# Performance work log

Measured on AMD Instinct MI355X. Metric: run time of the kernel, lower is better.

Reference implementation:

```python
import jax, jax.numpy as jnp
import numpy as np
from jax.scipy.special import digamma

# Dims (see init_kwargs): pose P=4 -> D=16, stem A=128, primary caps B=32,
# classes C=10, class-caps kernel K=6 (== primary feature map size), 3 routing iters.
P, D, A, B, C, K, ITER = 4, 16, 128, 32, 10, 6, 3
N = B * K * K                                    # input capsules routed to each class capsule
ALPHA0, KAPPA0, NU0 = 1.0, 1.0, float(D + 1)     # Dirichlet/Normal-Wishart priors (m0=0, Psi0=I, cov='diag')
BN_EPS, EPS = 1e-5, 1e-8


def conv2d(x, w, s):
    return jax.lax.conv_general_dilated(x, w, (s, s), 'VALID',
                                        dimension_numbers=('NCHW', 'OIHW', 'NCHW'))


def bn(x, gamma, beta, axes):
    # batch-norm with batch statistics (training-mode math)
    mu = x.mean(axes, keepdims=True)
    var = x.var(axes, keepdims=True)
    return (x - mu) * jax.lax.rsqrt(var + BN_EPS) * gamma + beta


def setup_inputs():
    key = jax.random.key(0)
    ks = jax.random.split(key, 4)
    f32 = jnp.float32
    x = jax.random.normal(ks[0], (128, 3, 32, 32), dtype=f32)
    conv1_w = jax.random.normal(ks[1], (A, 3, 5, 5), dtype=f32) * 0.1
    bn1_g = jnp.ones((A,), f32); bn1_b = jnp.zeros((A,), f32)
    prim_w = jax.random.normal(ks[2], (B * D + B, A, 3, 3), dtype=f32) * 0.05
    bna_g = jnp.ones((B,), f32); bna_b = jnp.zeros((B,), f32)
    bnp_g = jnp.ones((B,), f32); bnp_b = jnp.zeros((B,), f32)
    W_ij = jax.random.normal(ks[3], (B, C, K, K, P, P), dtype=f32) * 0.3
    return dict(x=x, conv1_w=conv1_w, bn1_g=bn1_g, bn1_b=bn1_b, prim_w=prim_w,
                bna_g=bna_g, bna_b=bna_b, bnp_g=bnp_g, bnp_b=bnp_b, W_ij=W_ij)


def _vb_stats(Ra, V):
    # Ra: (b,N,C) responsibility * input activation; V: (b,N,C,D) votes
    Nj = Ra.sum(1) + EPS                                         # (b,C)
    xbar = jnp.einsum('bnc,bncd->bcd', Ra, V) / Nj[..., None]    # weighted vote mean
    diff = V - xbar[:, None]
    sigma = jnp.einsum('bnc,bncd->bcd', Ra, diff * diff) / Nj[..., None]  # diag cov
    kappa = KAPPA0 + Nj
    m = Nj[..., None] * xbar / kappa[..., None]                  # posterior mean (m0 = 0)
    nu = NU0 + Nj
    Psi = 1.0 + Nj[..., None] * sigma + (KAPPA0 * Nj / kappa)[..., None] * xbar * xbar  # Psi0 = I (diag)
    return Nj, kappa, m, nu, Psi


def _expectations(Nj, nu, Psi, d_idx):
    alpha = ALPHA0 + Nj
    E_lnpi = digamma(alpha) - digamma(alpha.sum(-1, keepdims=True))
    E_lnLam = (digamma(0.5 * (nu[..., None] + 1.0 - d_idx)).sum(-1)
               + D * jnp.log(2.0) - jnp.log(Psi).sum(-1))
    return E_lnpi, E_lnLam


def reference(x, conv1_w, bn1_g, bn1_b, prim_w, bna_g, bna_b, bnp_g, bnp_b, W_ij):
    b = x.shape[0]
    # --- stem: Conv5x5/s2 + BN + ReLU ---
    h = conv2d(x, conv1_w, 2)                                    # (b,A,14,14)
    h = jax.nn.relu(bn(h, bn1_g[None, :, None, None], bn1_b[None, :, None, None], (0, 2, 3)))
    # --- primary capsules: Conv3x3/s2 -> poses + activations ---
    pc = conv2d(h, prim_w, 2)                                    # (b,B*D+B,6,6)
    poses, a = pc[:, :B * D], pc[:, B * D:]
    a = jax.nn.sigmoid(bn(a, bna_g[None, :, None, None], bna_b[None, :, None, None], (0, 2, 3)))
    poses = bn(poses.reshape(b, B, D, K, K),
               bnp_g[None, :, None, None, None], bnp_b[None, :, None, None, None], (0, 2, 3, 4))
    poses = poses.reshape(b, B, P, P, K, K)
    # --- class capsules: votes V = W_ij @ pose, kernel covers whole 6x6 map ---
    V = jnp.einsum('icxypq,biqrxy->bicxypr', W_ij, poses)        # (b,B,C,K,K,P,P)
    V = V.transpose(0, 1, 3, 4, 2, 5, 6).reshape(b, N, C, D)
    a_i = a.reshape(b, N)
    # --- variational Bayes routing (diag Normal-Wishart, ITER iterations) ---
    d_idx = jnp.arange(1, D + 1, dtype=x.dtype)
    R = jnp.full((b, N, C), 1.0 / C, dtype=x.dtype)
    for t in range(ITER):
        Nj, kappa, m, nu, Psi = _vb_stats(R * a_i[:, :, None], V)
        if t < ITER - 1:
            E_lnpi, E_lnLam = _expectations(Nj, nu, Psi, d_idx)
            dm = V - m[:, None]
            quad = D / kappa[:, None, :] + nu[:, None, :] * jnp.einsum('bncd,bcd->bnc', dm * dm, 1.0 / Psi)
            lnp = (E_lnpi[:, None] + 0.5 * E_lnLam[:, None]
                   - 0.5 * D * jnp.log(2.0 * jnp.pi) - 0.5 * quad)
            R = jax.nn.softmax(lnp, axis=-1)
    E_lnpi, E_lnLam = _expectations(Nj, nu, Psi, d_idx)
    logits = E_lnpi + 0.5 * E_lnLam                              # (b,C)
    yhat = jax.nn.sigmoid(bn(logits, 1.0, 0.0, (0,)))            # BatchNorm1d(affine=False)
    return yhat
```

## Files before the change

### kernel.cpp

```cpp
#include <hip/hip_runtime.h>
#include <hip/hip_bf16.h>

#define NB 128
#define AA 128
#define BB 32
#define CC 10
#define KK 6
#define DD 16
#define NN 1152
#define H1 14
#define CH2 544
#define NG 4608
#define KG 1152
#define MG 576

typedef short bfrag8 __attribute__((ext_vector_type(8)));
typedef float facc4 __attribute__((ext_vector_type(4)));

__device__ __forceinline__ unsigned short f2bf(float f) {
    unsigned u = __float_as_uint(f);
    u += 0x7FFF + ((u >> 16) & 1);
    return (unsigned short)(u >> 16);
}
__device__ __forceinline__ float bf2f(unsigned short s) {
    return __uint_as_float(((unsigned)s) << 16);
}

__global__ __launch_bounds__(256, 3) void k_conv1(const float* __restrict__ x,
                                                  const float* __restrict__ w,
                                                  float* __restrict__ h) {
    __shared__ __align__(16) float sX[3][7][32];
    __shared__ float sWf[AA * 75];
    const int p = blockIdx.x;
    const int b = blockIdx.y;
    const int tid = threadIdx.x;
    for (int j = tid; j < AA * 75; j += 256) sWf[j] = w[j];
    for (int j = tid; j < 3 * 7 * 32; j += 256) {
        int col = j & 31; int t2 = j >> 5; int row = t2 % 7; int ic = t2 / 7;
        sX[ic][row][col] = x[b * 3072 + ic * 1024 + (4 * p + row) * 32 + col];
    }
    __syncthreads();
    const int oc = tid & 127, ry = tid >> 7;
    const int r = 2 * p + ry;
    float acc[14];
#pragma unroll
    for (int j = 0; j < 14; ++j) acc[j] = 0.f;
    const float* wr = sWf + oc * 75;
#pragma unroll
    for (int ic = 0; ic < 3; ++ic) {
#pragma unroll
        for (int ky = 0; ky < 5; ++ky) {
            const float* xr = &sX[ic][2 * ry + ky][0];
            float row[32];
#pragma unroll
            for (int q = 0; q < 8; ++q) {
                float4 v = *reinterpret_cast<const float4*>(xr + q * 4);
                row[q * 4 + 0] = v.x; row[q * 4 + 1] = v.y;
                row[q * 4 + 2] = v.z; row[q * 4 + 3] = v.w;
            }
            float w0 = wr[ic * 25 + ky * 5 + 0];
            float w1 = wr[ic * 25 + ky * 5 + 1];
            float w2 = wr[ic * 25 + ky * 5 + 2];
            float w3 = wr[ic * 25 + ky * 5 + 3];
            float w4 = wr[ic * 25 + ky * 5 + 4];
#pragma unroll
            for (int ox = 0; ox < 14; ++ox) {
                float s = acc[ox];
                s = fmaf(row[2 * ox + 0], w0, s);
                s = fmaf(row[2 * ox + 1], w1, s);
                s = fmaf(row[2 * ox + 2], w2, s);
                s = fmaf(row[2 * ox + 3], w3, s);
                s = fmaf(row[2 * ox + 4], w4, s);
                acc[ox] = s;
            }
        }
    }
    float* out = h + ((size_t)(b * AA + oc) * 14 + r) * 14;
#pragma unroll
    for (int q = 0; q < 7; ++q)
        *reinterpret_cast<float2*>(out + q * 2) = make_float2(acc[q * 2], acc[q * 2 + 1]);
}

__device__ __forceinline__ void blk_reduce2(float& s, float& s2, int tid) {
#pragma unroll
    for (int o = 32; o > 0; o >>= 1) { s += __shfl_down(s, o); s2 += __shfl_down(s2, o); }
    __shared__ float ls[4], lq[4];
    int lane = tid & 63, wid = tid >> 6;
    if (lane == 0) { ls[wid] = s; lq[wid] = s2; }
    __syncthreads();
    if (tid == 0) {
        s = ls[0] + ls[1] + ls[2] + ls[3];
        s2 = lq[0] + lq[1] + lq[2] + lq[3];
    }
}

__global__ void k_bnstats1a(const float* __restrict__ h, float* __restrict__ part) {
    int c = blockIdx.x & 127, sl = blockIdx.x >> 7;
    int tid = threadIdx.x;
    float s = 0.f, s2 = 0.f;
    for (int j = tid; j < 16 * 196; j += 256) {
        int b = sl * 16 + j / 196, hw = j % 196;
        float v = h[((size_t)b * AA + c) * 196 + hw];
        s += v; s2 += v * v;
    }
    blk_reduce2(s, s2, tid);
    if (tid == 0) { part[c * 8 + sl] = s; part[1024 + c * 8 + sl] = s2; }
}

__global__ void k_bnfin1(const float* __restrict__ part, const float* __restrict__ g,
                         const float* __restrict__ be, float* __restrict__ bn1) {
    int c = threadIdx.x;
    float s = 0.f, s2 = 0.f;
#pragma unroll
    for (int sl = 0; sl < 8; ++sl) { s += part[c * 8 + sl]; s2 += part[1024 + c * 8 + sl]; }
    const float n = (float)(NB * 196);
    float mu = s / n;
    float var = s2 / n - mu * mu;
    float sc = g[c] * rsqrtf(var + 1e-5f);
    bn1[c] = sc;
    bn1[AA + c] = be[c] - mu * sc;
}

__global__ void k_prepw(const float* __restrict__ w, unsigned short* __restrict__ Ah,
                        unsigned short* __restrict__ Al) {
    int t = blockIdx.x * 256 + threadIdx.x;
    if (t >= MG * (KG / 8)) return;
    int row = t / (KG / 8), seg = t % (KG / 8);
    alignas(16) unsigned short hi[8], lo[8];
    if (row < CH2) {
        const float* src = w + (size_t)row * KG + seg * 8;
#pragma unroll
        for (int j = 0; j < 8; ++j) {
            float v = src[j];
            unsigned short hh = f2bf(v);
            hi[j] = hh;
            lo[j] = f2bf(v - bf2f(hh));
        }
    } else {
#pragma unroll
        for (int j = 0; j < 8; ++j) { hi[j] = 0; lo[j] = 0; }
    }
    *reinterpret_cast<uint4*>(Ah + (size_t)row * KG + seg * 8) = *reinterpret_cast<const uint4*>(hi);
    *reinterpret_cast<uint4*>(Al + (size_t)row * KG + seg * 8) = *reinterpret_cast<const uint4*>(lo);
}

__global__ void k_im2col(const float* __restrict__ h, const float* __restrict__ bn1,
                         unsigned short* __restrict__ Bh, unsigned short* __restrict__ Bl) {
    int t = blockIdx.x * 256 + threadIdx.x;
    if (t >= NG * (KG / 8)) return;
    int n = t / (KG / 8), seg = t % (KG / 8);
    int b = n / 36, xy = n % 36;
    int oy = xy / 6, ox = xy % 6;
    const float* hb = h + (size_t)b * (AA * 196) + (2 * oy) * 14 + 2 * ox;
    alignas(16) unsigned short hi[8], lo[8];
#pragma unroll
    for (int j = 0; j < 8; ++j) {
        int k = seg * 8 + j;
        int ic = k / 9, kk = k - ic * 9;
        int ky = kk / 3, kx = kk - ky * 3;
        float v = hb[ic * 196 + ky * 14 + kx];
        v = fmaxf(fmaf(v, bn1[ic], bn1[AA + ic]), 0.f);
        unsigned short hh = f2bf(v);
        hi[j] = hh;
        lo[j] = f2bf(v - bf2f(hh));
    }
    *reinterpret_cast<uint4*>(Bh + (size_t)n * KG + seg * 8) = *reinterpret_cast<const uint4*>(hi);
    *reinterpret_cast<uint4*>(Bl + (size_t)n * KG + seg * 8) = *reinterpret_cast<const uint4*>(lo);
}

__global__ __launch_bounds__(256, 4) void k_gemm(const unsigned short* __restrict__ Ah,
                                                 const unsigned short* __restrict__ Al,
                                                 const unsigned short* __restrict__ Bh,
                                                 const unsigned short* __restrict__ Bl,
                                                 float* __restrict__ pcT) {
    __shared__ alignas(16) unsigned short sAh[64][44], sAl[64][44];
    __shared__ alignas(16) unsigned short sBh[64][44], sBl[64][44];
    const int s = blockIdx.x;
    const int k8 = s & 7, j = s >> 3;
    const int jm = j / 9;
    const int y = k8 + 8 * jm;
    const int xg = j - 9 * jm;
    const int oc0 = xg * 64;
    const int n0 = y * 64;
    const int tid = threadIdx.x;
    const int lane = tid & 63, wv = tid >> 6;
    const int wm = wv >> 1, wn = wv & 1;
    const int quad = lane >> 4, r16 = lane & 15;
    const int srow = tid >> 2, sseg = tid & 3;

    facc4 acc[2][2] = {};
    const size_t gA = (size_t)(oc0 + srow) * KG + sseg * 8;
    const size_t gB = (size_t)(n0 + srow) * KG + sseg * 8;

    for (int ks = 0; ks < KG / 32; ++ks) {
        const int k0 = ks * 32;
        uint4 vAh = *reinterpret_cast<const uint4*>(Ah + gA + k0);
        uint4 vAl = *reinterpret_cast<const uint4*>(Al + gA + k0);
        uint4 vBh = *reinterpret_cast<const uint4*>(Bh + gB + k0);
        uint4 vBl = *reinterpret_cast<const uint4*>(Bl + gB + k0);
        __syncthreads();
        *reinterpret_cast<uint4*>(&sAh[srow][sseg * 8]) = vAh;
        *reinterpret_cast<uint4*>(&sAl[srow][sseg * 8]) = vAl;
        *reinterpret_cast<uint4*>(&sBh[srow][sseg * 8]) = vBh;
        *reinterpret_cast<uint4*>(&sBl[srow][sseg * 8]) = vBl;
        __syncthreads();
        bfrag8 ah[2], al[2], bh[2], bl[2];
#pragma unroll
        for (int i = 0; i < 2; ++i) {
            ah[i] = *reinterpret_cast<const bfrag8*>(&sAh[wm * 32 + i * 16 + r16][quad * 8]);
            al[i] = *reinterpret_cast<const bfrag8*>(&sAl[wm * 32 + i * 16 + r16][quad * 8]);
            bh[i] = *reinterpret_cast<const bfrag8*>(&sBh[wn * 32 + i * 16 + r16][quad * 8]);
            bl[i] = *reinterpret_cast<const bfrag8*>(&sBl[wn * 32 + i * 16 + r16][quad * 8]);
        }
#pragma unroll
        for (int i = 0; i < 2; ++i)
#pragma unroll
            for (int jj = 0; jj < 2; ++jj) {
                acc[i][jj] = __builtin_amdgcn_mfma_f32_16x16x32_bf16(ah[i], bh[jj], acc[i][jj], 0, 0, 0);
                acc[i][jj] = __builtin_amdgcn_mfma_f32_16x16x32_bf16(ah[i], bl[jj], acc[i][jj], 0, 0, 0);
                acc[i][jj] = __builtin_amdgcn_mfma_f32_16x16x32_bf16(al[i], bh[jj], acc[i][jj], 0, 0, 0);
            }
    }
#pragma unroll
    for (int i = 0; i < 2; ++i) {
        int oc_base = oc0 + wm * 32 + i * 16 + quad * 4;
        if (oc_base >= CH2) continue;
#pragma unroll
        for (int jj = 0; jj < 2; ++jj) {
            int n = n0 + wn * 32 + jj * 16 + r16;
            *reinterpret_cast<facc4*>(pcT + (size_t)n * CH2 + oc_base) = acc[i][jj];
        }
    }
}

__global__ void k_bnstats2a(const float* __restrict__ pcT, float* __restrict__ part) {
    int blk = blockIdx.x, tid = threadIdx.x;
    float s = 0.f, s2 = 0.f;
    if (blk < 256) {
        int i = blk >> 3, sl = blk & 7;
        for (int j = tid; j < 576 * 4; j += 256) {
            int row = sl * 576 + (j >> 2), q = j & 3;
            float4 v = *reinterpret_cast<const float4*>(pcT + (size_t)row * CH2 + i * 16 + q * 4);
            s += v.x + v.y + v.z + v.w;
            s2 += v.x * v.x + v.y * v.y + v.z * v.z + v.w * v.w;
        }
        blk_reduce2(s, s2, tid);
        if (tid == 0) { part[blk] = s; part[256 + blk] = s2; }
    } else {
        int t2 = blk - 256;
        int ch = t2 >> 1, sl = t2 & 1;
        for (int j = tid; j < 2304; j += 256) {
            int row = sl * 2304 + j;
            float v = pcT[(size_t)row * CH2 + BB * DD + ch];
            s += v; s2 += v * v;
        }
        blk_reduce2(s, s2, tid);
        if (tid == 0) { part[512 + t2] = s; part[576 + t2] = s2; }
    }
}

__global__ void k_bnfin2(const float* __restrict__ part,
                         const float* __restrict__ bna_g, const float* __restrict__ bna_b,
                         const float* __restrict__ bnp_g, const float* __restrict__ bnp_b,
                         float* __restrict__ bn2) {
    int t = threadIdx.x;
    if (t < 32) {
        float s = 0.f, s2 = 0.f;
#pragma unroll
        for (int sl = 0; sl < 8; ++sl) { s += part[t * 8 + sl]; s2 += part[256 + t * 8 + sl]; }
        const float n = (float)(NB * DD * 36);
        float mu = s / n, var = s2 / n - mu * mu;
        float sc = bnp_g[t] * rsqrtf(var + 1e-5f);
        bn2[t] = sc; bn2[32 + t] = bnp_b[t] - mu * sc;
    } else {
        int ch = t - 32;
        float s = part[512 + ch * 2] + part[512 + ch * 2 + 1];
        float s2 = part[576 + ch * 2] + part[576 + ch * 2 + 1];
        const float n = (float)(NB * 36);
        float mu = s / n, var = s2 / n - mu * mu;
        float sc = bna_g[ch] * rsqrtf(var + 1e-5f);
        bn2[64 + ch] = sc; bn2[96 + ch] = bna_b[ch] - mu * sc;
    }
}

template <int FIRST>
__global__ __launch_bounds__(640) void k_routed(
    const float* __restrict__ pcT, const float* __restrict__ bn2,
    const float* __restrict__ Wij, const float* __restrict__ m,
    const float* __restrict__ G, const float* __restrict__ base,
    float* __restrict__ S0p, float* __restrict__ S1p, float* __restrict__ S2p) {
    const int b = blockIdx.x >> 1, half = blockIdx.x & 1;
    const int tid = threadIdx.x;
    const int c = tid >> 6, lane = tid & 63;
    __shared__ float sLnp[2][CC][65];
    __shared__ float sBn2[128];
    if (tid < 128) sBn2[tid] = bn2[tid];
    float mc[16], Gc[16], basec = 0.f;
    if (!FIRST) {
        int bc16 = (b * CC + c) * 16;
#pragma unroll
        for (int d = 0; d < 16; ++d) { mc[d] = m[bc16 + d]; Gc[d] = G[bc16 + d]; }
        basec = base[b * CC + c];
    }
    float s0 = 0.f, s1[16], s2[16];
#pragma unroll
    for (int d = 0; d < 16; ++d) { s1[d] = 0.f; s2[d] = 0.f; }
    __syncthreads();

#pragma unroll 1
    for (int it = 0; it < 9; ++it) {
        const int n = half * 576 + it * 64 + lane;
        const int i = n / 36, xy = n - i * 36;
        const int row = b * 36 + xy;
        const float4* pp = reinterpret_cast<const float4*>(pcT + (size_t)row * CH2 + i * 16);
        const float4* wp = reinterpret_cast<const float4*>(Wij + (((size_t)i * CC + c) * 36 + xy) * 16);
        alignas(16) float P[16], W[16];
        *reinterpret_cast<float4*>(&P[0])  = pp[0];
        *reinterpret_cast<float4*>(&P[4])  = pp[1];
        *reinterpret_cast<float4*>(&P[8])  = pp[2];
        *reinterpret_cast<float4*>(&P[12]) = pp[3];
        *reinterpret_cast<float4*>(&W[0])  = wp[0];
        *reinterpret_cast<float4*>(&W[4])  = wp[1];
        *reinterpret_cast<float4*>(&W[8])  = wp[2];
        *reinterpret_cast<float4*>(&W[12]) = wp[3];
        const float psc = sBn2[i], psh = sBn2[32 + i];
#pragma unroll
        for (int d = 0; d < 16; ++d) P[d] = fmaf(P[d], psc, psh);
        float V[16];
#pragma unroll
        for (int p = 0; p < 4; ++p)
#pragma unroll
            for (int r = 0; r < 4; ++r)
                V[p * 4 + r] = W[p * 4 + 0] * P[0 + r] + W[p * 4 + 1] * P[4 + r] +
                               W[p * 4 + 2] * P[8 + r] + W[p * 4 + 3] * P[12 + r];
        float va = fmaf(pcT[(size_t)row * CH2 + BB * DD + i], sBn2[64 + i], sBn2[96 + i]);
        float av = 1.f / (1.f + expf(-va));
        float wgt;
        if (FIRST) {
            wgt = 0.1f * av;
        } else {
            float q = 0.f;
#pragma unroll
            for (int d = 0; d < 16; ++d) {
                float dm = V[d] - mc[d];
                q = fmaf(dm * dm, Gc[d], q);
            }
            float lnp = basec - q;
            sLnp[it & 1][c][lane] = lnp;
            __syncthreads();
            float mx = -1e30f;
#pragma unroll
            for (int cc = 0; cc < CC; ++cc) mx = fmaxf(mx, sLnp[it & 1][cc][lane]);
            float ssum = 0.f;
#pragma unroll
            for (int cc = 0; cc < CC; ++cc) ssum += expf(sLnp[it & 1][cc][lane] - mx);
            wgt = expf(lnp - mx) / ssum * av;
        }
        s0 += wgt;
#pragma unroll
        for (int d = 0; d < 16; ++d) {
            float wv = wgt * V[d];
            s1[d] += wv;
            s2[d] = fmaf(wv, V[d], s2[d]);
        }
    }
#pragma unroll
    for (int o = 32; o > 0; o >>= 1) {
        s0 += __shfl_down(s0, o);
#pragma unroll
        for (int k = 0; k < 16; ++k) {
            s1[k] += __shfl_down(s1[k], o);
            s2[k] += __shfl_down(s2[k], o);
        }
    }
    if (lane == 0) {
        int idx = half * (NB * CC) + b * CC + c;
        S0p[idx] = s0;
#pragma unroll
        for (int k = 0; k < 16; ++k) { S1p[idx * 16 + k] = s1[k]; S2p[idx * 16 + k] = s2[k]; }
    }
}

__device__ __forceinline__ float digammaf_(float x) {
    float r = 0.f;
    while (x < 6.f) { r -= 1.f / x; x += 1.f; }
    float xi = 1.f / x;
    float xi2 = xi * xi;
    return r + logf(x) - 0.5f * xi -
           xi2 * (0.0833333333f - xi2 * (0.0083333333f - xi2 * 0.0039682540f));
}

template <int LOGITS>
__global__ void k_expect(const float* __restrict__ S0p, const float* __restrict__ S1p,
                         const float* __restrict__ S2p, float* __restrict__ m,
                         float* __restrict__ G, float* __restrict__ base,
                         float* __restrict__ logits) {
    int b = blockIdx.x;
    int c = threadIdx.x;
    __shared__ float alph[CC];
    float njraw = 0.f;
    if (c < CC) {
        njraw = S0p[b * CC + c] + S0p[NB * CC + b * CC + c];
        alph[c] = 1.f + njraw + 1e-8f;
    }
    __syncthreads();
    if (c < CC) {
        int bc = b * CC + c;
        float nj = njraw + 1e-8f;
        float asum = 0.f;
#pragma unroll
        for (int k = 0; k < CC; ++k) asum += alph[k];
        float kappa = 1.f + nj;
        float nu = 17.f + nj;
        float S0 = njraw;
        float elnlam = 16.f * 0.69314718056f;
        for (int d = 0; d < 16; ++d) {
            float s1 = S1p[bc * 16 + d] + S1p[(NB * CC + bc) * 16 + d];
            float s2v = S2p[bc * 16 + d] + S2p[(NB * CC + bc) * 16 + d];
            float xbar = s1 / nj;
            float sig = (s2v - 2.f * xbar * s1 + xbar * xbar * S0) / nj;
            float Psi = 1.f + nj * sig + (nj / kappa) * xbar * xbar;
            elnlam += digammaf_(0.5f * (nu + 1.f - (float)(d + 1))) - logf(Psi);
            m[bc * 16 + d] = nj * xbar / kappa;
            G[bc * 16 + d] = 0.5f * nu / Psi;
        }
        float elnpi = digammaf_(1.f + nj) - digammaf_(asum);
        float lb = elnpi + 0.5f * elnlam;
        if (LOGITS) logits[bc] = lb;
        base[bc] = lb - 8.f * 1.83787706641f - 8.f / kappa;
    }
}

__global__ void k_final(const float* __restrict__ logits, float* __restrict__ out) {
    int c = blockIdx.x;
    int b = threadIdx.x;
    float v = logits[b * CC + c];
    float s = v, s2 = v * v;
#pragma unroll
    for (int o = 32; o > 0; o >>= 1) { s += __shfl_down(s, o); s2 += __shfl_down(s2, o); }
    __shared__ float ls[2], lq[2];
    int lane = b & 63, wid = b >> 6;
    if (lane == 0) { ls[wid] = s; lq[wid] = s2; }
    __syncthreads();
    float mu = (ls[0] + ls[1]) * (1.f / 128.f);
    float var = (lq[0] + lq[1]) * (1.f / 128.f) - mu * mu;
    out[b * CC + c] = 1.f / (1.f + expf(-(v - mu) * rsqrtf(var + 1e-5f)));
}

extern "C" void kernel_launch(void* const* d_in, const int* in_sizes, int n_in,
                              void* d_out, int out_size, void* d_ws, size_t ws_size,
                              hipStream_t stream) {
    (void)in_sizes; (void)n_in; (void)out_size; (void)ws_size;
    const float* x       = (const float*)d_in[0];
    const float* conv1_w = (const float*)d_in[1];
    const float* bn1_g   = (const float*)d_in[2];
    const float* bn1_b   = (const float*)d_in[3];
    const float* prim_w  = (const float*)d_in[4];
    const float* bna_g   = (const float*)d_in[5];
    const float* bna_b   = (const float*)d_in[6];
    const float* bnp_g   = (const float*)d_in[7];
    const float* bnp_b   = (const float*)d_in[8];
    const float* Wij     = (const float*)d_in[9];

    float* ws = (float*)d_ws;
    float* h   = ws;
    float* pcT = ws + 3211264;
    unsigned short* Bh = (unsigned short*)(ws + 5718016);
    unsigned short* Bl = (unsigned short*)(ws + 8372224);
    unsigned short* Ahp = (unsigned short*)(ws + 11026432);
    unsigned short* Alp = (unsigned short*)(ws + 11358208);
    float* bn1    = ws + 11689984;
    float* bn2    = ws + 11690240;
    float* S0p    = ws + 11690368;
    float* S1p    = ws + 11692928;
    float* S2p    = ws + 11733888;
    float* m      = ws + 11774848;
    float* G      = ws + 11795328;
    float* base   = ws + 11815808;
    float* logits = ws + 11817088;
    float* part1  = ws + 11818368;
    float* part2  = ws + 11820416;
    float* out    = (float*)d_out;

    k_conv1<<<dim3(7, 128), 256, 0, stream>>>(x, conv1_w, h);
    k_bnstats1a<<<1024, 256, 0, stream>>>(h, part1);
    k_bnfin1<<<1, 128, 0, stream>>>(part1, bn1_g, bn1_b, bn1);
    k_prepw<<<324, 256, 0, stream>>>(prim_w, Ahp, Alp);
    k_im2col<<<2592, 256, 0, stream>>>(h, bn1, Bh, Bl);
    k_gemm<<<648, 256, 0, stream>>>(Ahp, Alp, Bh, Bl, pcT);
    k_bnstats2a<<<320, 256, 0, stream>>>(pcT, part2);
    k_bnfin2<<<1, 64, 0, stream>>>(part2, bna_g, bna_b, bnp_g, bnp_b, bn2);

    k_routed<1><<<256, 640, 0, stream>>>(pcT, bn2, Wij, m, G, base, S0p, S1p, S2p);
    k_expect<0><<<128, 64, 0, stream>>>(S0p, S1p, S2p, m, G, base, logits);
    k_routed<0><<<256, 640, 0, stream>>>(pcT, bn2, Wij, m, G, base, S0p, S1p, S2p);
    k_expect<0><<<128, 64, 0, stream>>>(S0p, S1p, S2p, m, G, base, logits);
    k_routed<0><<<256, 640, 0, stream>>>(pcT, bn2, Wij, m, G, base, S0p, S1p, S2p);
    k_expect<1><<<128, 64, 0, stream>>>(S0p, S1p, S2p, m, G, base, logits);

    k_final<<<10, 128, 0, stream>>>(logits, out);
}
```

Baseline: 215.7 us.

## Fuse routing expectation step into routed kernel and share pose loads via LDS

The per-iteration expectation kernel is folded into the start of each routed kernel, which now recomputes m, G and base per block from the previous iteration's partial sums, using a 16-lane shuffle reduction and LDS. Partial-sum buffers are ping-ponged so no separate expect launch is needed between iterations. Pose and activation loads, along with their BN affine and sigmoid, are now done once per block and staged in shared memory instead of being repeated by all ten class waves. The cost is an extra barrier per loop iteration and some duplicated expectation math, since both half-blocks of each sample compute it.

New measurement: 188.0 us. 12.8% less time.

```diff
diff --git a/kernel.cpp b/kernel.cpp
--- a/kernel.cpp
+++ b/kernel.cpp
@@ -283,104 +283,6 @@
     }
 }
 
-template <int FIRST>
-__global__ __launch_bounds__(640) void k_routed(
-    const float* __restrict__ pcT, const float* __restrict__ bn2,
-    const float* __restrict__ Wij, const float* __restrict__ m,
-    const float* __restrict__ G, const float* __restrict__ base,
-    float* __restrict__ S0p, float* __restrict__ S1p, float* __restrict__ S2p) {
-    const int b = blockIdx.x >> 1, half = blockIdx.x & 1;
-    const int tid = threadIdx.x;
-    const int c = tid >> 6, lane = tid & 63;
-    __shared__ float sLnp[2][CC][65];
-    __shared__ float sBn2[128];
-    if (tid < 128) sBn2[tid] = bn2[tid];
-    float mc[16], Gc[16], basec = 0.f;
-    if (!FIRST) {
-        int bc16 = (b * CC + c) * 16;
-#pragma unroll
-        for (int d = 0; d < 16; ++d) { mc[d] = m[bc16 + d]; Gc[d] = G[bc16 + d]; }
-        basec = base[b * CC + c];
-    }
-    float s0 = 0.f, s1[16], s2[16];
-#pragma unroll
-    for (int d = 0; d < 16; ++d) { s1[d] = 0.f; s2[d] = 0.f; }
-    __syncthreads();
-
-#pragma unroll 1
-    for (int it = 0; it < 9; ++it) {
-        const int n = half * 576 + it * 64 + lane;
-        const int i = n / 36, xy = n - i * 36;
-        const int row = b * 36 + xy;
-        const float4* pp = reinterpret_cast<const float4*>(pcT + (size_t)row * CH2 + i * 16);
-        const float4* wp = reinterpret_cast<const float4*>(Wij + (((size_t)i * CC + c) * 36 + xy) * 16);
-        alignas(16) float P[16], W[16];
-        *reinterpret_cast<float4*>(&P[0])  = pp[0];
-        *reinterpret_cast<float4*>(&P[4])  = pp[1];
-        *reinterpret_cast<float4*>(&P[8])  = pp[2];
-        *reinterpret_cast<float4*>(&P[12]) = pp[3];
-        *reinterpret_cast<float4*>(&W[0])  = wp[0];
-        *reinterpret_cast<float4*>(&W[4])  = wp[1];
-        *reinterpret_cast<float4*>(&W[8])  = wp[2];
-        *reinterpret_cast<float4*>(&W[12]) = wp[3];
-        const float psc = sBn2[i], psh = sBn2[32 + i];
-#pragma unroll
-        for (int d = 0; d < 16; ++d) P[d] = fmaf(P[d], psc, psh);
-        float V[16];
-#pragma unroll
-        for (int p = 0; p < 4; ++p)
-#pragma unroll
-            for (int r = 0; r < 4; ++r)
-                V[p * 4 + r] = W[p * 4 + 0] * P[0 + r] + W[p * 4 + 1] * P[4 + r] +
-                               W[p * 4 + 2] * P[8 + r] + W[p * 4 + 3] * P[12 + r];
-        float va = fmaf(pcT[(size_t)row * CH2 + BB * DD + i], sBn2[64 + i], sBn2[96 + i]);
-        float av = 1.f / (1.f + expf(-va));
-        float wgt;
-        if (FIRST) {
-            wgt = 0.1f * av;
-        } else {
-            float q = 0.f;
-#pragma unroll
-            for (int d = 0; d < 16; ++d) {
-                float dm = V[d] - mc[d];
-                q = fmaf(dm * dm, Gc[d], q);
-            }
-            float lnp = basec - q;
-            sLnp[it & 1][c][lane] = lnp;
-            __syncthreads();
-            float mx = -1e30f;
-#pragma unroll
-            for (int cc = 0; cc < CC; ++cc) mx = fmaxf(mx, sLnp[it & 1][cc][lane]);
-            float ssum = 0.f;
-#pragma unroll
-            for (int cc = 0; cc < CC; ++cc) ssum += expf(sLnp[it & 1][cc][lane] - mx);
-            wgt = expf(lnp - mx) / ssum * av;
-        }
-        s0 += wgt;
-#pragma unroll
-        for (int d = 0; d < 16; ++d) {
-            float wv = wgt * V[d];
-            s1[d] += wv;
-            s2[d] = fmaf(wv, V[d], s2[d]);
-        }
-    }
-#pragma unroll
-    for (int o = 32; o > 0; o >>= 1) {
-        s0 += __shfl_down(s0, o);
-#pragma unroll
-        for (int k = 0; k < 16; ++k) {
-            s1[k] += __shfl_down(s1[k], o);
-            s2[k] += __shfl_down(s2[k], o);
-        }
-    }
-    if (lane == 0) {
-        int idx = half * (NB * CC) + b * CC + c;
-        S0p[idx] = s0;
-#pragma unroll
-        for (int k = 0; k < 16; ++k) { S1p[idx * 16 + k] = s1[k]; S2p[idx * 16 + k] = s2[k]; }
-    }
-}
-
 __device__ __forceinline__ float digammaf_(float x) {
     float r = 0.f;
     while (x < 6.f) { r -= 1.f / x; x += 1.f; }
@@ -390,11 +292,150 @@
            xi2 * (0.0833333333f - xi2 * (0.0083333333f - xi2 * 0.0039682540f));
 }
 
-template <int LOGITS>
-__global__ void k_expect(const float* __restrict__ S0p, const float* __restrict__ S1p,
-                         const float* __restrict__ S2p, float* __restrict__ m,
-                         float* __restrict__ G, float* __restrict__ base,
-                         float* __restrict__ logits) {
+template <int FIRST>
+__global__ __launch_bounds__(640) void k_routed(
+    const float* __restrict__ pcT, const float* __restrict__ bn2,
+    const float* __restrict__ Wij,
+    const float* __restrict__ S0i, const float* __restrict__ S1i, const float* __restrict__ S2i,
+    float* __restrict__ S0o, float* __restrict__ S1o, float* __restrict__ S2o) {
+    const int b = blockIdx.x >> 1, half = blockIdx.x & 1;
+    const int tid = threadIdx.x;
+    const int c = tid >> 6, lane = tid & 63;
+    __shared__ float sLnp[CC][66];
+    __shared__ float sBn2[128];
+    __shared__ __align__(16) float sP[64][20];
+    __shared__ float sA[64];
+    __shared__ float sM[CC][16], sGq[CC][16], sBase[CC];
+    if (tid < 128) sBn2[tid] = bn2[tid];
+    if (!FIRST && tid < 160) {
+        int cc = tid >> 4, d = tid & 15;
+        int bc = b * CC + cc;
+        float njraw = S0i[bc] + S0i[NB * CC + bc];
+        float nj = njraw + 1e-8f;
+        float kappa = 1.f + nj;
+        float nu = 17.f + nj;
+        float s1 = S1i[bc * 16 + d] + S1i[(NB * CC + bc) * 16 + d];
+        float s2v = S2i[bc * 16 + d] + S2i[(NB * CC + bc) * 16 + d];
+        float xbar = s1 / nj;
+        float sig = (s2v - 2.f * xbar * s1 + xbar * xbar * njraw) / nj;
+        float Psi = 1.f + nj * sig + (nj / kappa) * xbar * xbar;
+        sM[cc][d] = nj * xbar / kappa;
+        sGq[cc][d] = 0.5f * nu / Psi;
+        float term = digammaf_(0.5f * (nu + 1.f - (float)(d + 1))) - logf(Psi);
+#pragma unroll
+        for (int o = 8; o > 0; o >>= 1) term += __shfl_down(term, o, 16);
+        if (d == 0) {
+            float asum = 0.f;
+#pragma unroll
+            for (int k = 0; k < CC; ++k)
+                asum += 1.f + S0i[b * CC + k] + S0i[NB * CC + b * CC + k] + 1e-8f;
+            float elnlam = 16.f * 0.69314718056f + term;
+            float elnpi = digammaf_(1.f + nj) - digammaf_(asum);
+            float lb = elnpi + 0.5f * elnlam;
+            sBase[cc] = lb - 8.f * 1.83787706641f - 8.f / kappa;
+        }
+    }
+    __syncthreads();
+    float mc[16], Gc[16], basec = 0.f;
+    if (!FIRST) {
+#pragma unroll
+        for (int d = 0; d < 16; ++d) { mc[d] = sM[c][d]; Gc[d] = sGq[c][d]; }
+        basec = sBase[c];
+    }
+    float s0 = 0.f, s1[16], s2[16];
+#pragma unroll
+    for (int d = 0; d < 16; ++d) { s1[d] = 0.f; s2[d] = 0.f; }
+
+#pragma unroll 1
+    for (int it = 0; it < 9; ++it) {
+        if (tid < 256) {
+            int r = tid >> 2, q = tid & 3;
+            int n = half * 576 + it * 64 + r;
+            int i = n / 36, xy = n - i * 36;
+            int row = b * 36 + xy;
+            float4 v = *reinterpret_cast<const float4*>(pcT + (size_t)row * CH2 + i * 16 + q * 4);
+            float psc = sBn2[i], psh = sBn2[32 + i];
+            v.x = fmaf(v.x, psc, psh); v.y = fmaf(v.y, psc, psh);
+            v.z = fmaf(v.z, psc, psh); v.w = fmaf(v.w, psc, psh);
+            *reinterpret_cast<float4*>(&sP[r][q * 4]) = v;
+        } else if (tid < 320) {
+            int r = tid - 256;
+            int n = half * 576 + it * 64 + r;
+            int i = n / 36, xy = n - i * 36;
+            int row = b * 36 + xy;
+            float va = fmaf(pcT[(size_t)row * CH2 + BB * DD + i], sBn2[64 + i], sBn2[96 + i]);
+            sA[r] = 1.f / (1.f + expf(-va));
+        }
+        __syncthreads();
+        const int n = half * 576 + it * 64 + lane;
+        const int i = n / 36, xy = n - i * 36;
+        const float4* wp = reinterpret_cast<const float4*>(Wij + (((size_t)i * CC + c) * 36 + xy) * 16);
+        alignas(16) float P[16], W[16];
+        *reinterpret_cast<float4*>(&P[0])  = *reinterpret_cast<const float4*>(&sP[lane][0]);
+        *reinterpret_cast<float4*>(&P[4])  = *reinterpret_cast<const float4*>(&sP[lane][4]);
+        *reinterpret_cast<float4*>(&P[8])  = *reinterpret_cast<const float4*>(&sP[lane][8]);
+        *reinterpret_cast<float4*>(&P[12]) = *reinterpret_cast<const float4*>(&sP[lane][12]);
+        *reinterpret_cast<float4*>(&W[0])  = wp[0];
+        *reinterpret_cast<float4*>(&W[4])  = wp[1];
+        *reinterpret_cast<float4*>(&W[8])  = wp[2];
+        *reinterpret_cast<float4*>(&W[12]) = wp[3];
+        float V[16];
+#pragma unroll
+        for (int p = 0; p < 4; ++p)
+#pragma unroll
+            for (int r = 0; r < 4; ++r)
+                V[p * 4 + r] = W[p * 4 + 0] * P[0 + r] + W[p * 4 + 1] * P[4 + r] +
+                               W[p * 4 + 2] * P[8 + r] + W[p * 4 + 3] * P[12 + r];
+        float av = sA[lane];
+        float wgt;
+        if (FIRST) {
+            wgt = 0.1f * av;
+            __syncthreads();
+        } else {
+            float q = 0.f;
+#pragma unroll
+            for (int d = 0; d < 16; ++d) {
+                float dm = V[d] - mc[d];
+                q = fmaf(dm * dm, Gc[d], q);
+            }
+            float lnp = basec - q;
+            sLnp[c][lane] = lnp;
+            __syncthreads();
+            float mx = -1e30f;
+#pragma unroll
+            for (int cc = 0; cc < CC; ++cc) mx = fmaxf(mx, sLnp[cc][lane]);
+            float ssum = 0.f;
+#pragma unroll
+            for (int cc = 0; cc < CC; ++cc) ssum += expf(sLnp[cc][lane] - mx);
+            wgt = expf(lnp - mx) / ssum * av;
+        }
+        s0 += wgt;
+#pragma unroll
+        for (int d = 0; d < 16; ++d) {
+            float wv = wgt * V[d];
+            s1[d] += wv;
+            s2[d] = fmaf(wv, V[d], s2[d]);
+        }
+    }
+#pragma unroll
+    for (int o = 32; o > 0; o >>= 1) {
+        s0 += __shfl_down(s0, o);
+#pragma unroll
+        for (int k = 0; k < 16; ++k) {
+            s1[k] += __shfl_down(s1[k], o);
+            s2[k] += __shfl_down(s2[k], o);
+        }
+    }
+    if (lane == 0) {
+        int idx = half * (NB * CC) + b * CC + c;
+        S0o[idx] = s0;
+#pragma unroll
+        for (int k = 0; k < 16; ++k) { S1o[idx * 16 + k] = s1[k]; S2o[idx * 16 + k] = s2[k]; }
+    }
+}
+
+__global__ void k_expect_final(const float* __restrict__ S0p, const float* __restrict__ S1p,
+                               const float* __restrict__ S2p, float* __restrict__ logits) {
     int b = blockIdx.x;
     int c = threadIdx.x;
     __shared__ float alph[CC];
@@ -421,13 +462,9 @@
             float sig = (s2v - 2.f * xbar * s1 + xbar * xbar * S0) / nj;
             float Psi = 1.f + nj * sig + (nj / kappa) * xbar * xbar;
             elnlam += digammaf_(0.5f * (nu + 1.f - (float)(d + 1))) - logf(Psi);
-            m[bc * 16 + d] = nj * xbar / kappa;
-            G[bc * 16 + d] = 0.5f * nu / Psi;
         }
         float elnpi = digammaf_(1.f + nj) - digammaf_(asum);
-        float lb = elnpi + 0.5f * elnlam;
-        if (LOGITS) logits[bc] = lb;
-        base[bc] = lb - 8.f * 1.83787706641f - 8.f / kappa;
+        logits[bc] = elnpi + 0.5f * elnlam;
     }
 }
 
@@ -471,15 +508,15 @@
     unsigned short* Alp = (unsigned short*)(ws + 11358208);
     float* bn1    = ws + 11689984;
     float* bn2    = ws + 11690240;
-    float* S0p    = ws + 11690368;
-    float* S1p    = ws + 11692928;
-    float* S2p    = ws + 11733888;
-    float* m      = ws + 11774848;
-    float* G      = ws + 11795328;
-    float* base   = ws + 11815808;
-    float* logits = ws + 11817088;
-    float* part1  = ws + 11818368;
-    float* part2  = ws + 11820416;
+    float* S0a    = ws + 11690368;
+    float* S1a    = ws + 11692928;
+    float* S2a    = ws + 11733888;
+    float* S0b    = ws + 11774848;
+    float* S1b    = ws + 11777408;
+    float* S2b    = ws + 11818368;
+    float* logits = ws + 11859328;
+    float* part1  = ws + 11860608;
+    float* part2  = ws + 11862656;
     float* out    = (float*)d_out;
 
     k_conv1<<<dim3(7, 128), 256, 0, stream>>>(x, conv1_w, h);
@@ -491,12 +528,10 @@
     k_bnstats2a<<<320, 256, 0, stream>>>(pcT, part2);
     k_bnfin2<<<1, 64, 0, stream>>>(part2, bna_g, bna_b, bnp_g, bnp_b, bn2);
 
-    k_routed<1><<<256, 640, 0, stream>>>(pcT, bn2, Wij, m, G, base, S0p, S1p, S2p);
-    k_expect<0><<<128, 64, 0, stream>>>(S0p, S1p, S2p, m, G, base, logits);
-    k_routed<0><<<256, 640, 0, stream>>>(pcT, bn2, Wij, m, G, base, S0p, S1p, S2p);
-    k_expect<0><<<128, 64, 0, stream>>>(S0p, S1p, S2p, m, G, base, logits);
-    k_routed<0><<<256, 640, 0, stream>>>(pcT, bn2, Wij, m, G, base, S0p, S1p, S2p);
-    k_expect<1><<<128, 64, 0, stream>>>(S0p, S1p, S2p, m, G, base, logits);
+    k_routed<1><<<256, 640, 0, stream>>>(pcT, bn2, Wij, S0a, S1a, S2a, S0a, S1a, S2a);
+    k_routed<0><<<256, 640, 0, stream>>>(pcT, bn2, Wij, S0a, S1a, S2a, S0b, S1b, S2b);
+    k_routed<0><<<256, 640, 0, stream>>>(pcT, bn2, Wij, S0b, S1b, S2b, S0a, S1a, S2a);
+    k_expect_final<<<128, 64, 0, stream>>>(S0a, S1a, S2a, logits);
 
     k_final<<<10, 128, 0, stream>>>(logits, out);
 }
```
